# Optimization experiments

Hardware: AMD Instinct MI355X
Metric: run time of the kernel (lower is better)

The kernel has to match this reference:

```python
import jax, jax.numpy as jnp
import numpy as np

N_NODES = 40000
N_EDGES = 640000


def setup_inputs() -> dict:
    key = jax.random.key(0)
    ks = jax.random.split(key, 6)
    src_edges = jax.random.randint(ks[0], (N_EDGES,), 0, N_NODES, dtype=jnp.int32)
    dst_edges = jnp.sort(jax.random.randint(ks[1], (N_EDGES,), 0, N_NODES, dtype=jnp.int32))
    features = jax.random.normal(ks[2], (N_NODES, 128), dtype=jnp.float32)
    # GINConv.reset_parameters: uniform(-stdv, stdv), stdv = 1/sqrt(output_dim)
    def init_w(k, din, dout):
        stdv = 1.0 / np.sqrt(dout)
        return jax.random.uniform(k, (din, dout), jnp.float32, -stdv, stdv)
    W1 = init_w(ks[3], 128, 128)
    W2 = init_w(ks[4], 128, 128)
    W3 = init_w(ks[5], 128, 64)
    return {"src_edges": src_edges, "dst_edges": dst_edges, "features": features,
            "W1": W1, "W2": W2, "W3": W3}


def _gin_layer(h, src, dst, W):
    # gather src features [E, d], segment-sum into dst nodes, then linear
    agg = jax.ops.segment_sum(h[src], dst, num_segments=N_NODES)  # [N, d_in]
    return agg @ W  # [N, d_out]


def reference(src_edges, dst_edges, features, W1, W2, W3):
    src = src_edges.astype(jnp.int32)
    dst = dst_edges.astype(jnp.int32)
    h = _gin_layer(features, src, dst, W1)
    h = _gin_layer(h, src, dst, W2)  # dropout p=0.0 -> identity
    h = _gin_layer(h, src, dst, W3)
    return h
```

## Files before the change

### kernel.cpp

```cpp
#include <hip/hip_runtime.h>
#include <hip/hip_bf16.h>

#define N_NODES 40000
#define N_EDGES 640000

typedef __attribute__((ext_vector_type(8))) short bfrag;
typedef __attribute__((ext_vector_type(4))) float ffrag;

__device__ __forceinline__ float b2f_lo(unsigned u) {
    return __builtin_bit_cast(float, u << 16);
}
__device__ __forceinline__ float b2f_hi(unsigned u) {
    return __builtin_bit_cast(float, u & 0xffff0000u);
}
__device__ __forceinline__ unsigned short f2b(float f) {
    return __builtin_bit_cast(unsigned short, __float2bfloat16(f));
}

__global__ __launch_bounds__(256) void prepW(const float* __restrict__ W1,
                                             const float* __restrict__ W2,
                                             const float* __restrict__ W3,
                                             unsigned short* __restrict__ Wt123) {
    __shared__ float uS[4][128];
    const int wv   = threadIdx.x >> 6;
    const int lane = threadIdx.x & 63;
    const int k    = blockIdx.x * 4 + wv;

    float u0 = 0.f, u1 = 0.f;
    const float* w1p = W1 + k * 128;
    const float* w2p = W2 + 2 * lane;
#pragma unroll 8
    for (int j = 0; j < 128; j++) {
        float a  = w1p[j];
        float2 w = *(const float2*)(w2p + (size_t)j * 128);
        u0 += a * w.x;
        u1 += a * w.y;
    }
    uS[wv][2 * lane]     = u0;
    uS[wv][2 * lane + 1] = u1;
    __syncthreads();

    float acc = 0.f;
    const float* w3p = W3 + lane;
#pragma unroll 8
    for (int l = 0; l < 128; l++)
        acc += uS[wv][l] * w3p[(size_t)l * 64];
    Wt123[lane * 128 + k] = f2b(acc);
}

#define GEMM_BLOCKS 625
#define RP_BLOCKS   782
__global__ __launch_bounds__(256) void gemmR(const float* __restrict__ X,
                                             const unsigned short* __restrict__ Wt,
                                             unsigned short* __restrict__ Y,
                                             const int* __restrict__ dst,
                                             int* __restrict__ rowptr) {
    const int bid = blockIdx.x;
    if (bid >= GEMM_BLOCKS) {
        int i = (bid - GEMM_BLOCKS) * 256 + threadIdx.x;
        if (i < N_EDGES / 4) {
            int e = i * 4;
            int4 d4 = *(const int4*)(dst + e);
            int dp = (e == 0) ? -1 : dst[e - 1];
            for (int n = dp + 1;   n <= d4.x; n++) rowptr[n] = e;
            for (int n = d4.x + 1; n <= d4.y; n++) rowptr[n] = e + 1;
            for (int n = d4.y + 1; n <= d4.z; n++) rowptr[n] = e + 2;
            for (int n = d4.z + 1; n <= d4.w; n++) rowptr[n] = e + 3;
        } else if (i < N_EDGES / 4 + N_NODES + 1) {
            int n = i - N_EDGES / 4;
            if (n > dst[N_EDGES - 1]) rowptr[n] = N_EDGES;
        }
        return;
    }

    const int wv   = threadIdx.x >> 6;
    const int lane = threadIdx.x & 63;
    const int ml   = lane & 15;
    const int quad = lane >> 4;
    const int row0 = bid * 64 + wv * 16;

    ffrag acc[4];
#pragma unroll
    for (int c = 0; c < 4; c++) acc[c] = (ffrag)0.f;

#pragma unroll
    for (int kb = 0; kb < 128; kb += 32) {
        const float* p = X + (size_t)(row0 + ml) * 128 + kb + quad * 8;
        float4 u0 = *(const float4*)p;
        float4 u1 = *(const float4*)(p + 4);
        bfrag a;
        a[0] = (short)f2b(u0.x); a[1] = (short)f2b(u0.y);
        a[2] = (short)f2b(u0.z); a[3] = (short)f2b(u0.w);
        a[4] = (short)f2b(u1.x); a[5] = (short)f2b(u1.y);
        a[6] = (short)f2b(u1.z); a[7] = (short)f2b(u1.w);
#pragma unroll
        for (int c = 0; c < 4; c++) {
            const int col = c * 16 + ml;
            bfrag b = *(const bfrag*)(Wt + (size_t)col * 128 + kb + quad * 8);
            acc[c] = __builtin_amdgcn_mfma_f32_16x16x32_bf16(a, b, acc[c], 0, 0, 0);
        }
    }
#pragma unroll
    for (int c = 0; c < 4; c++)
#pragma unroll
        for (int i = 0; i < 4; i++)
            Y[(size_t)(row0 + quad * 4 + i) * 64 + c * 16 + ml] = f2b(acc[c][i]);
}

#define IDX_LDS 2048
template<bool OUT_F32>
__global__ __launch_bounds__(256) void scatter8(const unsigned short* __restrict__ T,
                                                const int* __restrict__ srcE,
                                                const int* __restrict__ rowptr,
                                                void* __restrict__ Hv) {
    __shared__ int shIdx[IDX_LDS];
    const int tid   = threadIdx.x;
    const int node0 = blockIdx.x * 32;
    const int ebase = rowptr[node0];
    const int etop  = rowptr[node0 + 32];
    const int total = etop - ebase;

    const int lim = total < IDX_LDS ? total : IDX_LDS;
    for (int j = tid; j < lim; j += 256) shIdx[j] = srcE[ebase + j];
    __syncthreads();

    const int lane = tid & 63;
    const int g    = lane >> 3;
    const int c8   = (lane & 7) * 8;
    const int node = node0 + (tid >> 6) * 8 + g;
    const int e0 = rowptr[node], e1 = rowptr[node + 1];

    float a0 = 0.f, a1 = 0.f, a2 = 0.f, a3 = 0.f;
    float a4 = 0.f, a5 = 0.f, a6 = 0.f, a7 = 0.f;

#define GATH(s) (*(const uint4*)(T + (size_t)(s) * 64 + c8))
#define ACCQ(t0, t1, t2, t3)                                                  \
    do {                                                                      \
        a0 += (b2f_lo(t0.x) + b2f_lo(t1.x)) + (b2f_lo(t2.x) + b2f_lo(t3.x));  \
        a1 += (b2f_hi(t0.x) + b2f_hi(t1.x)) + (b2f_hi(t2.x) + b2f_hi(t3.x));  \
        a2 += (b2f_lo(t0.y) + b2f_lo(t1.y)) + (b2f_lo(t2.y) + b2f_lo(t3.y));  \
        a3 += (b2f_hi(t0.y) + b2f_hi(t1.y)) + (b2f_hi(t2.y) + b2f_hi(t3.y));  \
        a4 += (b2f_lo(t0.z) + b2f_lo(t1.z)) + (b2f_lo(t2.z) + b2f_lo(t3.z));  \
        a5 += (b2f_hi(t0.z) + b2f_hi(t1.z)) + (b2f_hi(t2.z) + b2f_hi(t3.z));  \
        a6 += (b2f_lo(t0.w) + b2f_lo(t1.w)) + (b2f_lo(t2.w) + b2f_lo(t3.w));  \
        a7 += (b2f_hi(t0.w) + b2f_hi(t1.w)) + (b2f_hi(t2.w) + b2f_hi(t3.w));  \
    } while (0)

    int e = e0;
    if (total <= IDX_LDS) {
        uint4 A0, A1, A2, A3, B0, B1, B2, B3;
        bool haveA = false, haveB = false;
        if (e + 4 <= e1) {
            int o = e - ebase;
            A0 = GATH(shIdx[o]);     A1 = GATH(shIdx[o + 1]);
            A2 = GATH(shIdx[o + 2]); A3 = GATH(shIdx[o + 3]);
            e += 4; haveA = true;
            if (e + 4 <= e1) {
                o = e - ebase;
                B0 = GATH(shIdx[o]);     B1 = GATH(shIdx[o + 1]);
                B2 = GATH(shIdx[o + 2]); B3 = GATH(shIdx[o + 3]);
                e += 4; haveB = true;
            }
        }
        while (haveA) {
            ACCQ(A0, A1, A2, A3);
            if (e + 4 <= e1) {
                int o = e - ebase;
                A0 = GATH(shIdx[o]);     A1 = GATH(shIdx[o + 1]);
                A2 = GATH(shIdx[o + 2]); A3 = GATH(shIdx[o + 3]);
                e += 4;
            } else haveA = false;
            if (!haveB) break;
            ACCQ(B0, B1, B2, B3);
            if (e + 4 <= e1) {
                int o = e - ebase;
                B0 = GATH(shIdx[o]);     B1 = GATH(shIdx[o + 1]);
                B2 = GATH(shIdx[o + 2]); B3 = GATH(shIdx[o + 3]);
                e += 4;
            } else haveB = false;
        }
        const int rem = e1 - e;
        if (rem > 0) {
            int o = e - ebase;
            int s0 = shIdx[o];
            int s1 = (rem > 1) ? shIdx[o + 1] : s0;
            int s2 = (rem > 2) ? shIdx[o + 2] : s0;
            uint4 q0 = GATH(s0), q1 = GATH(s1), q2 = GATH(s2);
            a0 += b2f_lo(q0.x); a1 += b2f_hi(q0.x);
            a2 += b2f_lo(q0.y); a3 += b2f_hi(q0.y);
            a4 += b2f_lo(q0.z); a5 += b2f_hi(q0.z);
            a6 += b2f_lo(q0.w); a7 += b2f_hi(q0.w);
            if (rem > 1) {
                a0 += b2f_lo(q1.x); a1 += b2f_hi(q1.x);
                a2 += b2f_lo(q1.y); a3 += b2f_hi(q1.y);
                a4 += b2f_lo(q1.z); a5 += b2f_hi(q1.z);
                a6 += b2f_lo(q1.w); a7 += b2f_hi(q1.w);
            }
            if (rem > 2) {
                a0 += b2f_lo(q2.x); a1 += b2f_hi(q2.x);
                a2 += b2f_lo(q2.y); a3 += b2f_hi(q2.y);
                a4 += b2f_lo(q2.z); a5 += b2f_hi(q2.z);
                a6 += b2f_lo(q2.w); a7 += b2f_hi(q2.w);
            }
        }
    } else {
        uint4 t0, t1, t2, t3;
        bool have = (e + 4 <= e1);
        if (have) {
            int s0 = srcE[e], s1 = srcE[e + 1], s2 = srcE[e + 2], s3 = srcE[e + 3];
            t0 = GATH(s0); t1 = GATH(s1); t2 = GATH(s2); t3 = GATH(s3);
            e += 4;
        }
        while (have) {
            const bool next = (e + 4 <= e1);
            int s0, s1, s2, s3;
            if (next) { s0 = srcE[e]; s1 = srcE[e + 1]; s2 = srcE[e + 2]; s3 = srcE[e + 3]; }
            ACCQ(t0, t1, t2, t3);
            if (next) {
                t0 = GATH(s0); t1 = GATH(s1); t2 = GATH(s2); t3 = GATH(s3);
                e += 4;
            }
            have = next;
        }
        const int rem = e1 - e;
        if (rem > 0) {
            int s0 = srcE[e];
            int s1 = (rem > 1) ? srcE[e + 1] : s0;
            int s2 = (rem > 2) ? srcE[e + 2] : s0;
            uint4 q0 = GATH(s0), q1 = GATH(s1), q2 = GATH(s2);
            a0 += b2f_lo(q0.x); a1 += b2f_hi(q0.x);
            a2 += b2f_lo(q0.y); a3 += b2f_hi(q0.y);
            a4 += b2f_lo(q0.z); a5 += b2f_hi(q0.z);
            a6 += b2f_lo(q0.w); a7 += b2f_hi(q0.w);
            if (rem > 1) {
                a0 += b2f_lo(q1.x); a1 += b2f_hi(q1.x);
                a2 += b2f_lo(q1.y); a3 += b2f_hi(q1.y);
                a4 += b2f_lo(q1.z); a5 += b2f_hi(q1.z);
                a6 += b2f_lo(q1.w); a7 += b2f_hi(q1.w);
            }
            if (rem > 2) {
                a0 += b2f_lo(q2.x); a1 += b2f_hi(q2.x);
                a2 += b2f_lo(q2.y); a3 += b2f_hi(q2.y);
                a4 += b2f_lo(q2.z); a5 += b2f_hi(q2.z);
                a6 += b2f_lo(q2.w); a7 += b2f_hi(q2.w);
            }
        }
    }
#undef GATH
#undef ACCQ

    if constexpr (OUT_F32) {
        float* q = (float*)Hv + (size_t)node * 64 + c8;
        *(float4*)q       = make_float4(a0, a1, a2, a3);
        *(float4*)(q + 4) = make_float4(a4, a5, a6, a7);
    } else {
        ushort4 o0, o1;
        o0.x = f2b(a0); o0.y = f2b(a1); o0.z = f2b(a2); o0.w = f2b(a3);
        o1.x = f2b(a4); o1.y = f2b(a5); o1.z = f2b(a6); o1.w = f2b(a7);
        unsigned short* q = (unsigned short*)Hv + (size_t)node * 64 + c8;
        *(ushort4*)q       = o0;
        *(ushort4*)(q + 4) = o1;
    }
}

extern "C" void kernel_launch(void* const* d_in, const int* in_sizes, int n_in,
                              void* d_out, int out_size, void* d_ws, size_t ws_size,
                              hipStream_t stream) {
    const int*   src  = (const int*)d_in[0];
    const int*   dst  = (const int*)d_in[1];
    const float* feat = (const float*)d_in[2];
    const float* W1   = (const float*)d_in[3];
    const float* W2   = (const float*)d_in[4];
    const float* W3   = (const float*)d_in[5];
    float* out = (float*)d_out;

    char* wsb = (char*)d_ws;
    unsigned short* T     = (unsigned short*)wsb;
    unsigned short* H     = (unsigned short*)(wsb + (size_t)5505024);
    int* rowptr           = (int*)(wsb + (size_t)11010048);
    unsigned short* Wt123 = (unsigned short*)(wsb + (size_t)11010048 + 163968);

    const int scatterBlocks = (N_NODES + 31) / 32;

    prepW<<<32, 256, 0, stream>>>(W1, W2, W3, Wt123);
    gemmR<<<GEMM_BLOCKS + RP_BLOCKS, 256, 0, stream>>>(feat, Wt123, T, dst, rowptr);
    scatter8<false><<<scatterBlocks, 256, 0, stream>>>(T, src, rowptr, H);
    scatter8<false><<<scatterBlocks, 256, 0, stream>>>(H, src, rowptr, T);
    scatter8<true><<<scatterBlocks, 256, 0, stream>>>(T, src, rowptr, out);
}
```

Before: 134.4 us.

## Split feature columns into two halves mapped to separate XCD groups for L2 locality

The 64-column bf16 intermediate is split into two 32-column planes (lo/hi). Each scatter block handles one half, chosen from blockIdx modulo 8, so each group of XCDs gathers from a 2.56 MB table instead of a 5.1 MB one. The aim is to raise L2 hit rates on the random gathers. Blocks now cover 64 nodes with 4 lanes per node, and the LDS index buffer grows to 4096 entries. The fallback path for blocks with more edges than that becomes a simple unpipelined loop. The scheme assumes round-robin dispatch of blocks to XCDs, and it reads each index list twice, once per half.

```diff
diff --git a/kernel.cpp b/kernel.cpp
--- a/kernel.cpp
+++ b/kernel.cpp
@@ -52,7 +52,8 @@
 #define RP_BLOCKS   782
 __global__ __launch_bounds__(256) void gemmR(const float* __restrict__ X,
                                              const unsigned short* __restrict__ Wt,
-                                             unsigned short* __restrict__ Y,
+                                             unsigned short* __restrict__ Ylo,
+                                             unsigned short* __restrict__ Yhi,
                                              const int* __restrict__ dst,
                                              int* __restrict__ rowptr) {
     const int bid = blockIdx.x;
@@ -101,39 +102,50 @@
         }
     }
 #pragma unroll
-    for (int c = 0; c < 4; c++)
+    for (int c = 0; c < 4; c++) {
+        unsigned short* Yh = (c >= 2) ? Yhi : Ylo;
 #pragma unroll
         for (int i = 0; i < 4; i++)
-            Y[(size_t)(row0 + quad * 4 + i) * 64 + c * 16 + ml] = f2b(acc[c][i]);
-}
-
-#define IDX_LDS 2048
+            Yh[(size_t)(row0 + quad * 4 + i) * 32 + (c & 1) * 16 + ml] = f2b(acc[c][i]);
+    }
+}
+
+#define HIDX 4096
 template<bool OUT_F32>
-__global__ __launch_bounds__(256) void scatter8(const unsigned short* __restrict__ T,
+__global__ __launch_bounds__(256) void scatterS(const unsigned short* __restrict__ Tlo,
+                                                const unsigned short* __restrict__ Thi,
                                                 const int* __restrict__ srcE,
                                                 const int* __restrict__ rowptr,
-                                                void* __restrict__ Hv) {
-    __shared__ int shIdx[IDX_LDS];
+                                                void* __restrict__ Dlo,
+                                                void* __restrict__ Dhi) {
+    __shared__ int shIdx[HIDX];
+    const int bid   = blockIdx.x;
+    const int xcd   = bid & 7;
+    const int h     = xcd >> 2;
+    const int chunk = (bid >> 3) * 4 + (xcd & 3);
+    if (chunk >= 625) return;
+    const unsigned short* T = h ? Thi : Tlo;
+
     const int tid   = threadIdx.x;
-    const int node0 = blockIdx.x * 32;
+    const int node0 = chunk * 64;
     const int ebase = rowptr[node0];
-    const int etop  = rowptr[node0 + 32];
+    const int etop  = rowptr[node0 + 64];
     const int total = etop - ebase;
 
-    const int lim = total < IDX_LDS ? total : IDX_LDS;
+    const int lim = total < HIDX ? total : HIDX;
     for (int j = tid; j < lim; j += 256) shIdx[j] = srcE[ebase + j];
     __syncthreads();
 
     const int lane = tid & 63;
-    const int g    = lane >> 3;
-    const int c8   = (lane & 7) * 8;
-    const int node = node0 + (tid >> 6) * 8 + g;
+    const int g    = lane >> 2;
+    const int c8   = (lane & 3) * 8;
+    const int node = node0 + (tid >> 6) * 16 + g;
     const int e0 = rowptr[node], e1 = rowptr[node + 1];
 
     float a0 = 0.f, a1 = 0.f, a2 = 0.f, a3 = 0.f;
     float a4 = 0.f, a5 = 0.f, a6 = 0.f, a7 = 0.f;
 
-#define GATH(s) (*(const uint4*)(T + (size_t)(s) * 64 + c8))
+#define GATH(s) (*(const uint4*)(T + (size_t)(s) * 32 + c8))
 #define ACCQ(t0, t1, t2, t3)                                                  \
     do {                                                                      \
         a0 += (b2f_lo(t0.x) + b2f_lo(t1.x)) + (b2f_lo(t2.x) + b2f_lo(t3.x));  \
@@ -147,7 +159,7 @@
     } while (0)
 
     int e = e0;
-    if (total <= IDX_LDS) {
+    if (total <= HIDX) {
         uint4 A0, A1, A2, A3, B0, B1, B2, B3;
         bool haveA = false, haveB = false;
         if (e + 4 <= e1) {
@@ -204,60 +216,27 @@
             }
         }
     } else {
-        uint4 t0, t1, t2, t3;
-        bool have = (e + 4 <= e1);
-        if (have) {
-            int s0 = srcE[e], s1 = srcE[e + 1], s2 = srcE[e + 2], s3 = srcE[e + 3];
-            t0 = GATH(s0); t1 = GATH(s1); t2 = GATH(s2); t3 = GATH(s3);
-            e += 4;
-        }
-        while (have) {
-            const bool next = (e + 4 <= e1);
-            int s0, s1, s2, s3;
-            if (next) { s0 = srcE[e]; s1 = srcE[e + 1]; s2 = srcE[e + 2]; s3 = srcE[e + 3]; }
-            ACCQ(t0, t1, t2, t3);
-            if (next) {
-                t0 = GATH(s0); t1 = GATH(s1); t2 = GATH(s2); t3 = GATH(s3);
-                e += 4;
-            }
-            have = next;
-        }
-        const int rem = e1 - e;
-        if (rem > 0) {
-            int s0 = srcE[e];
-            int s1 = (rem > 1) ? srcE[e + 1] : s0;
-            int s2 = (rem > 2) ? srcE[e + 2] : s0;
-            uint4 q0 = GATH(s0), q1 = GATH(s1), q2 = GATH(s2);
-            a0 += b2f_lo(q0.x); a1 += b2f_hi(q0.x);
-            a2 += b2f_lo(q0.y); a3 += b2f_hi(q0.y);
-            a4 += b2f_lo(q0.z); a5 += b2f_hi(q0.z);
-            a6 += b2f_lo(q0.w); a7 += b2f_hi(q0.w);
-            if (rem > 1) {
-                a0 += b2f_lo(q1.x); a1 += b2f_hi(q1.x);
-                a2 += b2f_lo(q1.y); a3 += b2f_hi(q1.y);
-                a4 += b2f_lo(q1.z); a5 += b2f_hi(q1.z);
-                a6 += b2f_lo(q1.w); a7 += b2f_hi(q1.w);
-            }
-            if (rem > 2) {
-                a0 += b2f_lo(q2.x); a1 += b2f_hi(q2.x);
-                a2 += b2f_lo(q2.y); a3 += b2f_hi(q2.y);
-                a4 += b2f_lo(q2.z); a5 += b2f_hi(q2.z);
-                a6 += b2f_lo(q2.w); a7 += b2f_hi(q2.w);
-            }
+        for (int ee = e0; ee < e1; ee++) {
+            uint4 t0 = GATH(srcE[ee]);
+            a0 += b2f_lo(t0.x); a1 += b2f_hi(t0.x);
+            a2 += b2f_lo(t0.y); a3 += b2f_hi(t0.y);
+            a4 += b2f_lo(t0.z); a5 += b2f_hi(t0.z);
+            a6 += b2f_lo(t0.w); a7 += b2f_hi(t0.w);
         }
     }
 #undef GATH
 #undef ACCQ
 
     if constexpr (OUT_F32) {
-        float* q = (float*)Hv + (size_t)node * 64 + c8;
+        float* q = (float*)Dlo + (size_t)node * 64 + h * 32 + (lane & 3) * 8;
         *(float4*)q       = make_float4(a0, a1, a2, a3);
         *(float4*)(q + 4) = make_float4(a4, a5, a6, a7);
     } else {
         ushort4 o0, o1;
         o0.x = f2b(a0); o0.y = f2b(a1); o0.z = f2b(a2); o0.w = f2b(a3);
         o1.x = f2b(a4); o1.y = f2b(a5); o1.z = f2b(a6); o1.w = f2b(a7);
-        unsigned short* q = (unsigned short*)Hv + (size_t)node * 64 + c8;
+        unsigned short* q = (unsigned short*)(h ? Dhi : Dlo)
+                          + (size_t)node * 32 + (lane & 3) * 8;
         *(ushort4*)q       = o0;
         *(ushort4*)(q + 4) = o1;
     }
@@ -275,16 +254,18 @@
     float* out = (float*)d_out;
 
     char* wsb = (char*)d_ws;
-    unsigned short* T     = (unsigned short*)wsb;
-    unsigned short* H     = (unsigned short*)(wsb + (size_t)5505024);
-    int* rowptr           = (int*)(wsb + (size_t)11010048);
-    unsigned short* Wt123 = (unsigned short*)(wsb + (size_t)11010048 + 163968);
-
-    const int scatterBlocks = (N_NODES + 31) / 32;
+    unsigned short* Tlo   = (unsigned short*)wsb;
+    unsigned short* Thi   = (unsigned short*)(wsb + (size_t)2560000);
+    unsigned short* Hlo   = (unsigned short*)(wsb + (size_t)5120000);
+    unsigned short* Hhi   = (unsigned short*)(wsb + (size_t)7680000);
+    int* rowptr           = (int*)(wsb + (size_t)10240000);
+    unsigned short* Wt123 = (unsigned short*)(wsb + (size_t)10240000 + 160016);
+
+    const int scatterBlocks = 1280;
 
     prepW<<<32, 256, 0, stream>>>(W1, W2, W3, Wt123);
-    gemmR<<<GEMM_BLOCKS + RP_BLOCKS, 256, 0, stream>>>(feat, Wt123, T, dst, rowptr);
-    scatter8<false><<<scatterBlocks, 256, 0, stream>>>(T, src, rowptr, H);
-    scatter8<false><<<scatterBlocks, 256, 0, stream>>>(H, src, rowptr, T);
-    scatter8<true><<<scatterBlocks, 256, 0, stream>>>(T, src, rowptr, out);
-}
+    gemmR<<<GEMM_BLOCKS + RP_BLOCKS, 256, 0, stream>>>(feat, Wt123, Tlo, Thi, dst, rowptr);
+    scatterS<false><<<scatterBlocks, 256, 0, stream>>>(Tlo, Thi, src, rowptr, Hlo, Hhi);
+    scatterS<false><<<scatterBlocks, 256, 0, stream>>>(Hlo, Hhi, src, rowptr, Tlo, Thi);
+    scatterS<true><<<scatterBlocks, 256, 0, stream>>>(Tlo, Thi, src, rowptr, out, out);
+}
```

After: 135.4 us. No clear change (+0.7%).
